# Performance work log

Hardware: AMD Instinct MI355X
Metric: run time of the kernel (lower is better)

The kernel has to match this reference:

```python
import jax, jax.numpy as jnp
import numpy as np

B, S, D, H, E = 256, 256, 512, 512, 512


def setup_inputs() -> dict:
    key = jax.random.key(0)
    ks = jax.random.split(key, 12)
    inv = lambda n: 1.0 / np.sqrt(n)
    inp = {
        "prev_h": jax.random.normal(ks[0], (B, H), jnp.float32),
        "prev_c": jax.random.normal(ks[1], (B, H), jnp.float32),
        "batch_H": jax.random.normal(ks[2], (B, S, D), jnp.float32),
        "char_onehots": jax.nn.one_hot(jax.random.randint(ks[3], (B,), 0, E), E, dtype=jnp.float32),
        # parameters (torch nn.Linear convention: y = x @ W.T + b)
        "W_feat": jax.random.uniform(ks[4], (H, D), jnp.float32, -inv(D), inv(D)),
        "W_hid": jax.random.uniform(ks[5], (H, H), jnp.float32, -inv(H), inv(H)),
        "b_hid": jax.random.uniform(ks[6], (H,), jnp.float32, -inv(H), inv(H)),
        "w_score": jax.random.uniform(ks[7], (H,), jnp.float32, -inv(H), inv(H)),
        "W_ih": jax.random.uniform(ks[8], (4 * H, D + E), jnp.float32, -inv(H), inv(H)),
        "W_hh": jax.random.uniform(ks[9], (4 * H, H), jnp.float32, -inv(H), inv(H)),
        "b_ih": jax.random.uniform(ks[10], (4 * H,), jnp.float32, -inv(H), inv(H)),
        "b_hh": jax.random.uniform(ks[11], (4 * H,), jnp.float32, -inv(H), inv(H)),
    }
    return inp


def reference(prev_h, prev_c, batch_H, char_onehots, W_feat, W_hid, b_hid,
              w_score, W_ih, W_hh, b_ih, b_hh):
    # Bahdanau additive attention
    feat_proj = jnp.einsum('bsd,hd->bsh', batch_H, W_feat)            # [B,S,H]
    hidden_proj = prev_h @ W_hid.T + b_hid                            # [B,H]
    energies = jnp.tanh(feat_proj + hidden_proj[:, None, :]) @ w_score  # [B,S]
    alpha = jax.nn.softmax(energies, axis=1)                          # [B,S]
    context = jnp.einsum('bs,bsd->bd', alpha, batch_H)                # [B,D]
    # LSTMCell step (torch gate order: i, f, g, o)
    x = jnp.concatenate([context, char_onehots], axis=1)              # [B,D+E]
    gates = x @ W_ih.T + b_ih + prev_h @ W_hh.T + b_hh                # [B,4H]
    i, f, g, o = jnp.split(gates, 4, axis=1)
    c_new = jax.nn.sigmoid(f) * prev_c + jax.nn.sigmoid(i) * jnp.tanh(g)
    h_new = jax.nn.sigmoid(o) * jnp.tanh(c_new)
    return h_new, c_new, alpha
```

## Files before the change

### kernel.cpp

```cpp
#include <hip/hip_runtime.h>
#include <hip/hip_bf16.h>

typedef unsigned short u16;
typedef unsigned int u32;
typedef __attribute__((ext_vector_type(8))) short bf16x8;
typedef __attribute__((ext_vector_type(4))) float f32x4;
typedef __attribute__((ext_vector_type(4))) u32 u32x4;

typedef __attribute__((address_space(1))) const void gvoid;
typedef __attribute__((address_space(3))) void svoid;

__device__ __forceinline__ void gload16(const void* g, void* l) {
  __builtin_amdgcn_global_load_lds((gvoid*)g, (svoid*)l, 16, 0, 0);
}

__device__ __forceinline__ u16 f2bf(float x){
  union { float f; unsigned u; } v; v.f = x;
  unsigned r = v.u + 0x7fffu + ((v.u >> 16) & 1u);
  return (u16)(r >> 16);
}
__device__ __forceinline__ u32 pack_trunc(float a, float b){
  union { float f; u32 u; } ua, ub; ua.f = a; ub.f = b;
  return __builtin_amdgcn_perm(ub.u, ua.u, 0x07060302u);
}
__device__ __forceinline__ float fast_tanh(float x){
  x = fminf(fmaxf(x, -12.f), 12.f);
  float e = __expf(2.f * x);
  return (e - 1.f) / (e + 1.f);
}
__device__ __forceinline__ float fast_sig(float x){
  return 1.f / (1.f + __expf(-x));
}

__global__ __launch_bounds__(256) void prep_kernel(
    const float* __restrict__ Wfeat, const float* __restrict__ Whid,
    const float* __restrict__ Wih,   const float* __restrict__ Whh,
    const float* __restrict__ onehot,const float* __restrict__ prevh,
    const float* __restrict__ bih,   const float* __restrict__ bhh,
    u16* __restrict__ wfeat_b, u16* __restrict__ whid_b,
    u16* __restrict__ wcat, u16* __restrict__ xh, float* __restrict__ biascat)
{
  int idx = (blockIdx.x * 256 + threadIdx.x) * 4;
  const float* src;
  u16* dst;
  if (idx < 262144) { src = Wfeat + idx; dst = wfeat_b + idx; }
  else if ((idx -= 262144) < 262144) { src = Whid + idx; dst = whid_b + idx; }
  else if ((idx -= 262144) < 2097152) {
    int r = idx >> 10, k = idx & 1023; src = Wih + idx; dst = wcat + r*1536 + k;
  }
  else if ((idx -= 2097152) < 1048576) {
    int r = idx >> 9, k = idx & 511; src = Whh + idx; dst = wcat + r*1536 + 1024 + k;
  }
  else if ((idx -= 1048576) < 131072) {
    int b = idx >> 9, e = idx & 511; src = onehot + idx; dst = xh + b*1536 + 512 + e;
  }
  else if ((idx -= 131072) < 131072) {
    int b = idx >> 9, h = idx & 511; src = prevh + idx; dst = xh + b*1536 + 1024 + h;
  }
  else {
    idx -= 131072;
    if (idx < 2048) {
      float4 a = *(const float4*)(bih + idx);
      float4 b = *(const float4*)(bhh + idx);
      float4 c = { a.x + b.x, a.y + b.y, a.z + b.z, a.w + b.w };
      *(float4*)(biascat + idx) = c;
    }
    return;
  }
  float4 v = *(const float4*)src;
  ushort4 u;
  u.x = f2bf(v.x); u.y = f2bf(v.y); u.z = f2bf(v.z); u.w = f2bf(v.w);
  *(ushort4*)dst = u;
}

__global__ __launch_bounds__(256) void gemm_btk(
    const u16* __restrict__ Ab, int lda,
    const u16* __restrict__ Wb, int ldw,
    int ksteps, int pstride,
    float* __restrict__ P, int ldc)
{
  __shared__ u16 sA[128][40];
  __shared__ u16 sW[128][40];
  const int tid = threadIdx.x;
  const int lane = tid & 63, wave = tid >> 6;
  const int wr = wave >> 1, wc = wave & 1;
  const int lr = lane & 15, kg = lane >> 4;
  const int m0 = blockIdx.x * 128, n0 = blockIdx.y * 128;
  const int kbase = blockIdx.z * ksteps * 32;
  P += (size_t)blockIdx.z * pstride;
  const int sr = tid >> 1, sh = tid & 1;

  const f32x4 zero = {0.f, 0.f, 0.f, 0.f};
  f32x4 acc[4][4];
  #pragma unroll
  for (int i = 0; i < 4; ++i)
    #pragma unroll
    for (int j = 0; j < 4; ++j)
      acc[i][j] = zero;

  for (int ks = 0; ks < ksteps; ++ks) {
    const int kt = kbase + ks * 32;
    __syncthreads();
    {
      const u16* ap = Ab + (size_t)(m0 + sr) * lda + kt + sh * 16;
      *(bf16x8*)&sA[sr][sh*16]     = *(const bf16x8*)ap;
      *(bf16x8*)&sA[sr][sh*16 + 8] = *(const bf16x8*)(ap + 8);
      const u16* wp = Wb + (size_t)(n0 + sr) * ldw + kt + sh * 16;
      *(bf16x8*)&sW[sr][sh*16]     = *(const bf16x8*)wp;
      *(bf16x8*)&sW[sr][sh*16 + 8] = *(const bf16x8*)(wp + 8);
    }
    __syncthreads();
    bf16x8 af[4], wf[4];
    #pragma unroll
    for (int mi = 0; mi < 4; ++mi) af[mi] = *(const bf16x8*)&sA[wr*64 + mi*16 + lr][kg*8];
    #pragma unroll
    for (int ni = 0; ni < 4; ++ni) wf[ni] = *(const bf16x8*)&sW[wc*64 + ni*16 + lr][kg*8];
    #pragma unroll
    for (int mi = 0; mi < 4; ++mi)
      #pragma unroll
      for (int ni = 0; ni < 4; ++ni)
        acc[mi][ni] = __builtin_amdgcn_mfma_f32_16x16x32_bf16(af[mi], wf[ni], acc[mi][ni], 0, 0, 0);
  }

  #pragma unroll
  for (int ni = 0; ni < 4; ++ni) {
    const int col = n0 + wc*64 + ni*16 + lr;
    #pragma unroll
    for (int mi = 0; mi < 4; ++mi) {
      const int row = m0 + wr*64 + mi*16 + kg*4;
      #pragma unroll
      for (int rr = 0; rr < 4; ++rr)
        P[(size_t)(row + rr) * ldc + col] = acc[mi][ni][rr];
    }
  }
}

__global__ __launch_bounds__(512, 4) void energies_gemm(
    const float* __restrict__ A, const u16* __restrict__ Wb,
    const float* __restrict__ hpp, const float* __restrict__ bhid,
    const float* __restrict__ wsc, float* __restrict__ epart)
{
  __shared__ u16 sA[2][128 * 32];
  __shared__ u16 sW[2][256 * 32];
  const int tid = threadIdx.x;
  const int lane = tid & 63, wv = tid >> 6;
  const int wr = wv >> 2, wc = wv & 3;
  const int lr = lane & 15, kg = lane >> 4;
  const int m0 = blockIdx.x * 128, n0 = blockIdx.y * 256;
  const int b = m0 >> 8;

  const int arow = tid >> 2, achk = tid & 3;
  const float* gA = A + (size_t)(m0 + arow) * 512 + achk * 8;
  const int adst = arow * 32 + ((achk ^ ((arow >> 1) & 3)) * 8);

  const u16* gW0 = Wb + (size_t)(n0 + wv * 16 + (lane >> 2)) * 512 + (lane & 3) * 8;
  const u16* gW1 = gW0 + 128 * 512;
  const int wdst0 = wv * 1024;
  const int wdst1 = wdst0 + 4096;

  const f32x4 zero = {0.f, 0.f, 0.f, 0.f};
  f32x4 acc[4][4];
  #pragma unroll
  for (int i = 0; i < 4; ++i)
    #pragma unroll
    for (int j = 0; j < 4; ++j)
      acc[i][j] = zero;

  float4 p0 = *(const float4*)(gA);
  float4 p1 = *(const float4*)(gA + 4);
  gload16(gW0, &sW[0][wdst0]);
  gload16(gW1, &sW[0][wdst1]);
  {
    u32x4 c;
    c[0] = pack_trunc(p0.x, p0.y); c[1] = pack_trunc(p0.z, p0.w);
    c[2] = pack_trunc(p1.x, p1.y); c[3] = pack_trunc(p1.z, p1.w);
    *(u32x4*)&sA[0][adst] = c;
  }
  __syncthreads();

  for (int t = 0; t < 16; ++t) {
    const int cur = t & 1, nxt = cur ^ 1;
    if (t < 15) {
      const int kt = (t + 1) * 32;
      p0 = *(const float4*)(gA + kt);
      p1 = *(const float4*)(gA + kt + 4);
      gload16(gW0 + kt, &sW[nxt][wdst0]);
      gload16(gW1 + kt, &sW[nxt][wdst1]);
    }
    bf16x8 af[4], wf[4];
    #pragma unroll
    for (int mi = 0; mi < 4; ++mi) {
      const int row = wr*64 + mi*16 + lr;
      af[mi] = *(const bf16x8*)&sA[cur][row * 32 + ((kg ^ ((row >> 1) & 3)) * 8)];
    }
    #pragma unroll
    for (int ni = 0; ni < 4; ++ni)
      wf[ni] = *(const bf16x8*)&sW[cur][(wc*64 + ni*16 + lr) * 32 + kg*8];
    #pragma unroll
    for (int mi = 0; mi < 4; ++mi)
      #pragma unroll
      for (int ni = 0; ni < 4; ++ni)
        acc[mi][ni] = __builtin_amdgcn_mfma_f32_16x16x32_bf16(af[mi], wf[ni], acc[mi][ni], 0, 0, 0);
    if (t < 15) {
      u32x4 c;
      c[0] = pack_trunc(p0.x, p0.y); c[1] = pack_trunc(p0.z, p0.w);
      c[2] = pack_trunc(p1.x, p1.y); c[3] = pack_trunc(p1.z, p1.w);
      *(u32x4*)&sA[nxt][adst] = c;
    }
    __syncthreads();
  }

  float hpv[4], wsv[4];
  #pragma unroll
  for (int ni = 0; ni < 4; ++ni) {
    const int col = n0 + wc*64 + ni*16 + lr;
    float h = bhid[col];
    #pragma unroll
    for (int z = 0; z < 4; ++z) h += hpp[z * 131072 + b * 512 + col];
    hpv[ni] = h;
    wsv[ni] = wsc[col];
  }
  const int p = blockIdx.y * 4 + wc;
  #pragma unroll
  for (int mi = 0; mi < 4; ++mi) {
    #pragma unroll
    for (int rr = 0; rr < 4; ++rr) {
      float s = 0.f;
      #pragma unroll
      for (int ni = 0; ni < 4; ++ni)
        s += fast_tanh(acc[mi][ni][rr] + hpv[ni]) * wsv[ni];
      s += __shfl_xor(s, 1, 64);
      s += __shfl_xor(s, 2, 64);
      s += __shfl_xor(s, 4, 64);
      s += __shfl_xor(s, 8, 64);
      if (lr == 0)
        epart[p * 65536 + m0 + wr*64 + mi*16 + kg*4 + rr] = s;
    }
  }
}

__global__ __launch_bounds__(256) void softctx_k(
    const float* __restrict__ epart, const float* __restrict__ H,
    float* __restrict__ alpha, u16* __restrict__ xh)
{
  const int bb = blockIdx.x, t = threadIdx.x;
  float e = 0.f;
  #pragma unroll
  for (int p = 0; p < 8; ++p) e += epart[p * 65536 + bb * 256 + t];
  float mx = e;
  #pragma unroll
  for (int o = 32; o >= 1; o >>= 1) mx = fmaxf(mx, __shfl_xor(mx, o, 64));
  __shared__ float sm[4], ss[4];
  if ((t & 63) == 0) sm[t >> 6] = mx;
  __syncthreads();
  mx = fmaxf(fmaxf(sm[0], sm[1]), fmaxf(sm[2], sm[3]));
  float ex = __expf(e - mx);
  float sum = ex;
  #pragma unroll
  for (int o = 32; o >= 1; o >>= 1) sum += __shfl_xor(sum, o, 64);
  if ((t & 63) == 0) ss[t >> 6] = sum;
  __syncthreads();
  sum = ss[0] + ss[1] + ss[2] + ss[3];
  const float av = ex / sum;
  alpha[bb * 256 + t] = av;
  __shared__ float sal[256];
  sal[t] = av;
  __syncthreads();
  const int q = t >> 6, c = t & 63;
  float a[8];
  #pragma unroll
  for (int j = 0; j < 8; ++j) a[j] = 0.f;
  const float* p = H + (size_t)bb * 131072 + c * 8;
  for (int s = q * 64; s < q * 64 + 64; ++s) {
    float4 v0 = *(const float4*)(p + (size_t)s * 512);
    float4 v1 = *(const float4*)(p + (size_t)s * 512 + 4);
    const float al = sal[s];
    a[0] = fmaf(al, v0.x, a[0]); a[1] = fmaf(al, v0.y, a[1]);
    a[2] = fmaf(al, v0.z, a[2]); a[3] = fmaf(al, v0.w, a[3]);
    a[4] = fmaf(al, v1.x, a[4]); a[5] = fmaf(al, v1.y, a[5]);
    a[6] = fmaf(al, v1.z, a[6]); a[7] = fmaf(al, v1.w, a[7]);
  }
  __shared__ float red[256][8];
  #pragma unroll
  for (int j = 0; j < 8; ++j) red[t][j] = a[j];
  __syncthreads();
  if (q == 0) {
    #pragma unroll
    for (int j = 0; j < 8; ++j) {
      float s = red[t][j] + red[t + 64][j] + red[t + 128][j] + red[t + 192][j];
      xh[bb * 1536 + c * 8 + j] = f2bf(s);
    }
  }
}

__global__ __launch_bounds__(256) void lstm_reduce(
    const float* __restrict__ P, const float* __restrict__ biascat,
    const float* __restrict__ prev_c, float* __restrict__ out)
{
  const int idx = blockIdx.x * 256 + threadIdx.x;
  const int b = idx >> 9, h = idx & 511;
  float gi = biascat[h], gf = biascat[512 + h], gg = biascat[1024 + h], go = biascat[1536 + h];
  #pragma unroll
  for (int z = 0; z < 4; ++z) {
    const float* q = P + (size_t)z * 524288 + (size_t)b * 2048;
    gi += q[h]; gf += q[512 + h]; gg += q[1024 + h]; go += q[1536 + h];
  }
  const float c = fast_sig(gf) * prev_c[idx] + fast_sig(gi) * fast_tanh(gg);
  out[idx] = fast_sig(go) * fast_tanh(c);
  out[131072 + idx] = c;
}

extern "C" void kernel_launch(void* const* d_in, const int* in_sizes, int n_in,
                              void* d_out, int out_size, void* d_ws, size_t ws_size,
                              hipStream_t stream) {
  const float* prev_h  = (const float*)d_in[0];
  const float* prev_c  = (const float*)d_in[1];
  const float* batch_H = (const float*)d_in[2];
  const float* onehot  = (const float*)d_in[3];
  const float* W_feat  = (const float*)d_in[4];
  const float* W_hid   = (const float*)d_in[5];
  const float* b_hid   = (const float*)d_in[6];
  const float* w_score = (const float*)d_in[7];
  const float* W_ih    = (const float*)d_in[8];
  const float* W_hh    = (const float*)d_in[9];
  const float* b_ih    = (const float*)d_in[10];
  const float* b_hh    = (const float*)d_in[11];
  float* out = (float*)d_out;

  char* ws = (char*)d_ws;
  u16*   wfeat_b = (u16*)(ws);
  u16*   whid_b  = (u16*)(ws + 524288);
  u16*   wcat    = (u16*)(ws + 1048576);
  u16*   xh      = (u16*)(ws + 7340032);
  float* biascat = (float*)(ws + 8126464);
  float* hpp     = (float*)(ws + 8134656);
  float* epart   = (float*)(ws + 10231808);
  float* gpart   = (float*)(ws + 12328960);

  float* alpha = out + 262144;

  prep_kernel<<<3842, 256, 0, stream>>>(W_feat, W_hid, W_ih, W_hh, onehot, prev_h,
                                        b_ih, b_hh, wfeat_b, whid_b, wcat, xh, biascat);
  gemm_btk<<<dim3(2, 4, 4), 256, 0, stream>>>(xh + 1024, 1536, whid_b, 512, 4, 131072, hpp, 512);
  energies_gemm<<<dim3(512, 2), 512, 0, stream>>>(batch_H, wfeat_b, hpp, b_hid, w_score, epart);
  softctx_k<<<256, 256, 0, stream>>>(epart, batch_H, alpha, xh);
  gemm_btk<<<dim3(2, 16, 4), 256, 0, stream>>>(xh, 1536, wcat, 1536, 12, 524288, gpart, 2048);
  lstm_reduce<<<512, 256, 0, stream>>>(gpart, biascat, prev_c, out);
}
```

Measured before the change: 127.2 us.

## Deepen A-operand prefetch to two stages and use packed bf16 convert

```diff
diff --git a/kernel.cpp b/kernel.cpp
--- a/kernel.cpp
+++ b/kernel.cpp
@@ -19,9 +19,10 @@
   unsigned r = v.u + 0x7fffu + ((v.u >> 16) & 1u);
   return (u16)(r >> 16);
 }
-__device__ __forceinline__ u32 pack_trunc(float a, float b){
-  union { float f; u32 u; } ua, ub; ua.f = a; ub.f = b;
-  return __builtin_amdgcn_perm(ub.u, ua.u, 0x07060302u);
+__device__ __forceinline__ u32 cvtpk(float lo, float hi){
+  u32 r;
+  asm("v_cvt_pk_bf16_f32 %0, %1, %2" : "=v"(r) : "v"(lo), "v"(hi));
+  return r;
 }
 __device__ __forceinline__ float fast_tanh(float x){
   x = fminf(fmaxf(x, -12.f), 12.f);
@@ -155,7 +156,7 @@
 
   const u16* gW0 = Wb + (size_t)(n0 + wv * 16 + (lane >> 2)) * 512 + (lane & 3) * 8;
   const u16* gW1 = gW0 + 128 * 512;
-  const int wdst0 = wv * 1024;
+  const int wdst0 = wv * 512;
   const int wdst1 = wdst0 + 4096;
 
   const f32x4 zero = {0.f, 0.f, 0.f, 0.f};
@@ -166,27 +167,39 @@
     for (int j = 0; j < 4; ++j)
       acc[i][j] = zero;
 
-  float4 p0 = *(const float4*)(gA);
-  float4 p1 = *(const float4*)(gA + 4);
+  float4 pa0, pa1, pb0, pb1;
+
   gload16(gW0, &sW[0][wdst0]);
   gload16(gW1, &sW[0][wdst1]);
+  __builtin_amdgcn_sched_barrier(0);
+  pa0 = *(const float4*)(gA);       pa1 = *(const float4*)(gA + 4);
+  pb0 = *(const float4*)(gA + 32);  pb1 = *(const float4*)(gA + 36);
+  __builtin_amdgcn_sched_barrier(0);
   {
     u32x4 c;
-    c[0] = pack_trunc(p0.x, p0.y); c[1] = pack_trunc(p0.z, p0.w);
-    c[2] = pack_trunc(p1.x, p1.y); c[3] = pack_trunc(p1.z, p1.w);
+    c[0] = cvtpk(pa0.x, pa0.y); c[1] = cvtpk(pa0.z, pa0.w);
+    c[2] = cvtpk(pa1.x, pa1.y); c[3] = cvtpk(pa1.z, pa1.w);
     *(u32x4*)&sA[0][adst] = c;
   }
-  __syncthreads();
-
+  asm volatile("s_waitcnt lgkmcnt(0)" ::: "memory");
+  __builtin_amdgcn_s_barrier();
+  __builtin_amdgcn_sched_barrier(0);
+
+  #pragma unroll
   for (int t = 0; t < 16; ++t) {
     const int cur = t & 1, nxt = cur ^ 1;
     if (t < 15) {
       const int kt = (t + 1) * 32;
-      p0 = *(const float4*)(gA + kt);
-      p1 = *(const float4*)(gA + kt + 4);
       gload16(gW0 + kt, &sW[nxt][wdst0]);
       gload16(gW1 + kt, &sW[nxt][wdst1]);
     }
+    __builtin_amdgcn_sched_barrier(0);
+    if (t < 14) {
+      const int kt = (t + 2) * 32;
+      if (t & 1) { pb0 = *(const float4*)(gA + kt); pb1 = *(const float4*)(gA + kt + 4); }
+      else       { pa0 = *(const float4*)(gA + kt); pa1 = *(const float4*)(gA + kt + 4); }
+    }
+    __builtin_amdgcn_sched_barrier(0);
     bf16x8 af[4], wf[4];
     #pragma unroll
     for (int mi = 0; mi < 4; ++mi) {
@@ -203,11 +216,22 @@
         acc[mi][ni] = __builtin_amdgcn_mfma_f32_16x16x32_bf16(af[mi], wf[ni], acc[mi][ni], 0, 0, 0);
     if (t < 15) {
       u32x4 c;
-      c[0] = pack_trunc(p0.x, p0.y); c[1] = pack_trunc(p0.z, p0.w);
-      c[2] = pack_trunc(p1.x, p1.y); c[3] = pack_trunc(p1.z, p1.w);
+      if (t & 1) {
+        c[0] = cvtpk(pa0.x, pa0.y); c[1] = cvtpk(pa0.z, pa0.w);
+        c[2] = cvtpk(pa1.x, pa1.y); c[3] = cvtpk(pa1.z, pa1.w);
+      } else {
+        c[0] = cvtpk(pb0.x, pb0.y); c[1] = cvtpk(pb0.z, pb0.w);
+        c[2] = cvtpk(pb1.x, pb1.y); c[3] = cvtpk(pb1.z, pb1.w);
+      }
       *(u32x4*)&sA[nxt][adst] = c;
     }
-    __syncthreads();
+    if (t < 15) {
+      if (t < 14) asm volatile("s_waitcnt vmcnt(2)" ::: "memory");
+      else        asm volatile("s_waitcnt vmcnt(0)" ::: "memory");
+      asm volatile("s_waitcnt lgkmcnt(0)" ::: "memory");
+      __builtin_amdgcn_s_barrier();
+      __builtin_amdgcn_sched_barrier(0);
+    }
   }
 
   float hpv[4], wsv[4];
```

After: 118.6 us. 6.8% less time.
